# Performance work log

Measured on AMD Instinct MI355X. Metric: run time of the kernel, lower is better.

## Reference

```python
import jax, jax.numpy as jnp
import numpy as np

VOCAB = 30522
PAD_ID = 1  # original skips token id 1


def masked_mean(emb, mask):
    # emb: [..., L, D], mask: [..., L] -> [..., D]
    m = mask.astype(emb.dtype)[..., None]
    s = jnp.sum(emb * m, axis=-2)
    c = jnp.clip(jnp.sum(m, axis=-2), 1.0)
    return s / c


def arg_embedding(tok_ids, sent_ids, emb):
    # tok_ids: [B,S,A,T] int, sent_ids: [B,S,L] int, emb: [B,S,L,D]
    # For each non-pad token: mean of embeddings at all matching sentence
    # positions (0 if no match); then mean over non-pad tokens (0 if none).
    matches = (tok_ids[..., None] == sent_ids[:, :, None, None, :]).astype(emb.dtype)  # [B,S,A,T,L]
    cnt = jnp.clip(jnp.sum(matches, axis=-1, keepdims=True), 1.0)                      # [B,S,A,T,1]
    valid = (tok_ids != PAD_ID).astype(emb.dtype)[..., None]                           # [B,S,A,T,1]
    W = jnp.sum(matches / cnt * valid, axis=3)                                         # [B,S,A,L]
    n_valid = jnp.clip(jnp.sum(valid, axis=(3, 4)), 1.0)[..., None]                    # [B,S,A,1]
    return jnp.einsum('bsal,bsld->bsad', W, emb) / n_valid                             # [B,S,A,D]


def setup_inputs() -> dict:
    key = jax.random.key(0)
    ks = jax.random.split(key, 6)
    B, S, L, D, A, T = 16, 16, 128, 768, 8, 8
    return {
        'sentence_ids': jax.random.randint(ks[0], (B, S, L), 0, VOCAB, dtype=jnp.int64) if jax.config.jax_enable_x64 else jax.random.randint(ks[0], (B, S, L), 0, VOCAB, dtype=jnp.int32),
        'sentence_attention_masks': jax.random.randint(ks[1], (B, S, L), 0, 2, dtype=jnp.int32),
        'sentence_embeddings': jax.random.normal(ks[2], (B, S, L, D), dtype=jnp.float32),
        'predicate_ids': jax.random.randint(ks[3], (B, S, A, T), 0, VOCAB, dtype=jnp.int32),
        'arg0_ids': jax.random.randint(ks[4], (B, S, A, T), 0, VOCAB, dtype=jnp.int32),
        'arg1_ids': jax.random.randint(ks[5], (B, S, A, T), 0, VOCAB, dtype=jnp.int32),
    }


def reference(sentence_ids, sentence_attention_masks, sentence_embeddings,
              predicate_ids, arg0_ids, arg1_ids):
    # sentence_embeddings stands in for bert_model(input_ids, attention_mask)[0]
    sentence_embeddings_avg = masked_mean(sentence_embeddings, sentence_attention_masks)  # [B,S,D]
    predicate_embeddings = arg_embedding(predicate_ids, sentence_ids, sentence_embeddings)
    arg0_embeddings = arg_embedding(arg0_ids, sentence_ids, sentence_embeddings)
    arg1_embeddings = arg_embedding(arg1_ids, sentence_ids, sentence_embeddings)
    return (sentence_embeddings_avg, predicate_embeddings, arg0_embeddings, arg1_embeddings)
```

## Files before the change

### kernel.cpp

```cpp
#include <hip/hip_runtime.h>

#define BB 16
#define SS 16
#define LL 128
#define DD 768
#define AA 8
#define TT 8
#define PAD_ID 1
#define NARG 24
#define NT 768
#define NQ 96
#define NSEG 8
#define SEGL 16
#define CH 2
#define COLS 384

__global__ __launch_bounds__(NT, 8) void srl_kernel(
    const int* __restrict__ sid_g,
    const int* __restrict__ mask_g,
    const float* __restrict__ emb_g,
    const int* __restrict__ pred_g,
    const int* __restrict__ a0_g,
    const int* __restrict__ a1_g,
    float* __restrict__ out)
{
    __shared__ int    sid[LL];
    __shared__ float  maskf[LL];
    __shared__ float  Wt4[LL][4];
    __shared__ float  coeff[NARG][TT];
    __shared__ float  validf[NARG][TT];
    __shared__ int    toks[NARG][TT];
    __shared__ float  inv_msum;
    __shared__ int    amask_sh;
    __shared__ int    nact_sh;
    __shared__ int    actlist[NARG];
    __shared__ int    slotmap[NARG];
    __shared__ float4 P4[NSEG][NQ][4];
    __shared__ float  Wx[LL];

    const int bs  = blockIdx.x;
    const int cc  = blockIdx.y;
    const int tid = threadIdx.x;
    const int q   = tid % NQ;
    const int seg = tid / NQ;

    float* out0 = out;
    float* outA = out + (size_t)BB * SS * DD;
    const int colbase = cc * COLS + 4 * q;

    const float* ep = emb_g + (size_t)bs * (LL * DD)
                    + (size_t)(seg * SEGL) * DD + colbase;
    float4 cur0 = *reinterpret_cast<const float4*>(&ep[0]);
    float4 cur1 = *reinterpret_cast<const float4*>(&ep[DD]);

    if (tid < LL) {
        sid[tid]   = sid_g[bs * LL + tid];
        maskf[tid] = (float)mask_g[bs * LL + tid];
    }
    if (tid == 0) amask_sh = 0;
    __syncthreads();

    if (tid < NARG * TT) {
        const int j = tid >> 3;
        const int t = tid & 7;
        const int k = j >> 3;
        const int a = j & 7;
        const int* src = (k == 0) ? pred_g : (k == 1) ? a0_g : a1_g;
        const int tok = src[bs * AA * TT + a * TT + t];
        int cnt = 0;
        for (int l = 0; l < LL; ++l) cnt += (sid[l] == tok) ? 1 : 0;
        const float v = (tok != PAD_ID) ? 1.0f : 0.0f;
        toks[j][t]   = tok;
        validf[j][t] = v;
        coeff[j][t]  = v / (float)(cnt > 1 ? cnt : 1);
        if (v != 0.0f && cnt > 0) atomicOr(&amask_sh, 1 << j);
    } else if (tid >= 320 && tid < 384) {
        const int lane = tid - 320;
        float s = maskf[lane] + maskf[lane + 64];
        for (int off = 32; off; off >>= 1) s += __shfl_xor(s, off, 64);
        if (lane == 0) inv_msum = 1.0f / fmaxf(s, 1.0f);
    }
    __syncthreads();

    if (tid < NARG) {
        float nv = 0.0f;
        #pragma unroll
        for (int t = 0; t < TT; ++t) nv += validf[tid][t];
        const float inv = 1.0f / fmaxf(nv, 1.0f);
        #pragma unroll
        for (int t = 0; t < TT; ++t) coeff[tid][t] *= inv;
    } else if (tid == NARG) {
        int n = 0;
        const int m = amask_sh;
        for (int j = 0; j < NARG; ++j) {
            slotmap[j] = -1;
            if ((m >> j) & 1) actlist[n++] = j;
        }
        nact_sh = n;
        for (int s = n; s < NARG; ++s) actlist[s] = -1;
        for (int s = 0; s < n && s < 3; ++s) slotmap[actlist[s]] = s + 1;
    }
    __syncthreads();

    if (tid < LL * 4) {
        const int l = tid >> 2;
        const int s = tid & 3;
        float w = 0.0f;
        if (s == 0) {
            w = maskf[l] * inv_msum;
        } else {
            const int j = actlist[s - 1];
            if (j >= 0) {
                const int sl = sid[l];
                #pragma unroll
                for (int t = 0; t < TT; ++t)
                    w += (sl == toks[j][t]) ? coeff[j][t] : 0.0f;
            }
        }
        Wt4[l][s] = w;
    }
    __syncthreads();

    float4 acc0 = make_float4(0.f, 0.f, 0.f, 0.f);
    float4 acc1 = acc0, acc2 = acc0, acc3 = acc0;
    {
        #pragma unroll
        for (int l0 = 0; l0 < SEGL; l0 += CH) {
            float4 nxt0, nxt1;
            if (l0 + CH < SEGL) {
                nxt0 = *reinterpret_cast<const float4*>(&ep[(size_t)(l0 + CH) * DD]);
                nxt1 = *reinterpret_cast<const float4*>(&ep[(size_t)(l0 + CH + 1) * DD]);
            }
            {
                const float4 w = *reinterpret_cast<const float4*>(&Wt4[seg * SEGL + l0][0]);
                const float4 e = cur0;
                acc0.x += w.x * e.x; acc0.y += w.x * e.y; acc0.z += w.x * e.z; acc0.w += w.x * e.w;
                acc1.x += w.y * e.x; acc1.y += w.y * e.y; acc1.z += w.y * e.z; acc1.w += w.y * e.w;
                acc2.x += w.z * e.x; acc2.y += w.z * e.y; acc2.z += w.z * e.z; acc2.w += w.z * e.w;
                acc3.x += w.w * e.x; acc3.y += w.w * e.y; acc3.z += w.w * e.z; acc3.w += w.w * e.w;
            }
            {
                const float4 w = *reinterpret_cast<const float4*>(&Wt4[seg * SEGL + l0 + 1][0]);
                const float4 e = cur1;
                acc0.x += w.x * e.x; acc0.y += w.x * e.y; acc0.z += w.x * e.z; acc0.w += w.x * e.w;
                acc1.x += w.y * e.x; acc1.y += w.y * e.y; acc1.z += w.y * e.z; acc1.w += w.y * e.w;
                acc2.x += w.z * e.x; acc2.y += w.z * e.y; acc2.z += w.z * e.z; acc2.w += w.z * e.w;
                acc3.x += w.w * e.x; acc3.y += w.w * e.y; acc3.z += w.w * e.z; acc3.w += w.w * e.w;
            }
            cur0 = nxt0;
            cur1 = nxt1;
        }
    }
    P4[seg][q][0] = acc0;
    P4[seg][q][1] = acc1;
    P4[seg][q][2] = acc2;
    P4[seg][q][3] = acc3;
    __syncthreads();

    {
        const int g = seg;
        #pragma unroll
        for (int i = 0; i < 4; ++i) {
            const int r = g + 8 * i;
            if (r >= 25) break;
            float4 val = make_float4(0.f, 0.f, 0.f, 0.f);
            int s = -1;
            if (r == 0) s = 0;
            else if (slotmap[r - 1] >= 0) s = slotmap[r - 1];
            if (s >= 0) {
                #pragma unroll
                for (int g2 = 0; g2 < NSEG; ++g2) {
                    const float4 p = P4[g2][q][s];
                    val.x += p.x; val.y += p.y; val.z += p.z; val.w += p.w;
                }
            }
            if (r == 0) {
                *reinterpret_cast<float4*>(&out0[(size_t)bs * DD + colbase]) = val;
            } else {
                const int j = r - 1;
                *reinterpret_cast<float4*>(
                    &outA[(size_t)(j >> 3) * (BB * SS * AA * DD) +
                          ((size_t)bs * AA + (j & 7)) * DD + colbase]) = val;
            }
        }
    }

    for (int e = 3; e < nact_sh; ++e) {
        const int je = actlist[e];
        __syncthreads();
        if (tid < LL) {
            const int sl = sid[tid];
            float w = 0.0f;
            #pragma unroll
            for (int t = 0; t < TT; ++t)
                w += (sl == toks[je][t]) ? coeff[je][t] : 0.0f;
            Wx[tid] = w;
        }
        __syncthreads();
        float4 acc = make_float4(0.f, 0.f, 0.f, 0.f);
        for (int l = 0; l < SEGL; ++l) {
            const float w = Wx[seg * SEGL + l];
            const float4 ev = *reinterpret_cast<const float4*>(&ep[(size_t)l * DD]);
            acc.x += w * ev.x; acc.y += w * ev.y; acc.z += w * ev.z; acc.w += w * ev.w;
        }
        P4[seg][q][0] = acc;
        __syncthreads();
        if (seg == 0) {
            float4 s = make_float4(0.f, 0.f, 0.f, 0.f);
            #pragma unroll
            for (int g2 = 0; g2 < NSEG; ++g2) {
                const float4 p = P4[g2][q][0];
                s.x += p.x; s.y += p.y; s.z += p.z; s.w += p.w;
            }
            *reinterpret_cast<float4*>(
                &outA[(size_t)(je >> 3) * (BB * SS * AA * DD) +
                      ((size_t)bs * AA + (je & 7)) * DD + colbase]) = s;
        }
    }
}

extern "C" void kernel_launch(void* const* d_in, const int* in_sizes, int n_in,
                              void* d_out, int out_size, void* d_ws, size_t ws_size,
                              hipStream_t stream) {
    const int*   sid  = (const int*)d_in[0];
    const int*   mask = (const int*)d_in[1];
    const float* emb  = (const float*)d_in[2];
    const int*   pred = (const int*)d_in[3];
    const int*   a0   = (const int*)d_in[4];
    const int*   a1   = (const int*)d_in[5];
    float* outp = (float*)d_out;

    srl_kernel<<<dim3(BB * SS, DD / COLS), dim3(NT), 0, stream>>>(
        sid, mask, emb, pred, a0, a1, outp);
}
```

Baseline: 29.20 us.

## Split into prep kernel computing weight rows and streaming weighted-sum kernel

Moves token matching, count and coefficient computation and the full weight matrix into a separate prep kernel that writes weights and an active-argument header to workspace. The streaming kernel then only reads precomputed weights and does the embedding accumulation. This removes the duplicated prep work that each column block did before, and it drops the serial prep phase from the bandwidth-bound kernel. The cost is a second launch plus a global round trip for the weights and header. The first kernel's embedding prefetch can no longer overlap the prep work.

After: 32.76 us. +12.2%, slower.

```diff
diff --git a/kernel.cpp b/kernel.cpp
--- a/kernel.cpp
+++ b/kernel.cpp
@@ -8,50 +8,35 @@
 #define TT 8
 #define PAD_ID 1
 #define NARG 24
-#define NT 768
+#define NROW 25
+#define NT1 384
+#define NT2 768
 #define NQ 96
 #define NSEG 8
 #define SEGL 16
-#define CH 2
 #define COLS 384
 
-__global__ __launch_bounds__(NT, 8) void srl_kernel(
+__global__ __launch_bounds__(NT1) void srl_prep(
     const int* __restrict__ sid_g,
     const int* __restrict__ mask_g,
-    const float* __restrict__ emb_g,
     const int* __restrict__ pred_g,
     const int* __restrict__ a0_g,
     const int* __restrict__ a1_g,
-    float* __restrict__ out)
+    float* __restrict__ Wfull,
+    int* __restrict__ hdr)
 {
-    __shared__ int    sid[LL];
-    __shared__ float  maskf[LL];
-    __shared__ float  Wt4[LL][4];
-    __shared__ float  coeff[NARG][TT];
-    __shared__ float  validf[NARG][TT];
-    __shared__ int    toks[NARG][TT];
-    __shared__ float  inv_msum;
-    __shared__ int    amask_sh;
-    __shared__ int    nact_sh;
-    __shared__ int    actlist[NARG];
-    __shared__ int    slotmap[NARG];
-    __shared__ float4 P4[NSEG][NQ][4];
-    __shared__ float  Wx[LL];
+    __shared__ int   sid[LL];
+    __shared__ float maskf[LL];
+    __shared__ float coeff[NARG][TT];
+    __shared__ float validf[NARG][TT];
+    __shared__ int   toks[NARG][TT];
+    __shared__ float inv_msum;
+    __shared__ int   amask_sh;
+    __shared__ int   nact_sh;
+    __shared__ int   actlist[NARG];
 
     const int bs  = blockIdx.x;
-    const int cc  = blockIdx.y;
     const int tid = threadIdx.x;
-    const int q   = tid % NQ;
-    const int seg = tid / NQ;
-
-    float* out0 = out;
-    float* outA = out + (size_t)BB * SS * DD;
-    const int colbase = cc * COLS + 4 * q;
-
-    const float* ep = emb_g + (size_t)bs * (LL * DD)
-                    + (size_t)(seg * SEGL) * DD + colbase;
-    float4 cur0 = *reinterpret_cast<const float4*>(&ep[0]);
-    float4 cur1 = *reinterpret_cast<const float4*>(&ep[DD]);
 
     if (tid < LL) {
         sid[tid]   = sid_g[bs * LL + tid];
@@ -92,64 +77,110 @@
     } else if (tid == NARG) {
         int n = 0;
         const int m = amask_sh;
-        for (int j = 0; j < NARG; ++j) {
-            slotmap[j] = -1;
+        for (int j = 0; j < NARG; ++j)
             if ((m >> j) & 1) actlist[n++] = j;
-        }
         nact_sh = n;
         for (int s = n; s < NARG; ++s) actlist[s] = -1;
-        for (int s = 0; s < n && s < 3; ++s) slotmap[actlist[s]] = s + 1;
-    }
-    __syncthreads();
+    }
+    __syncthreads();
+
+    for (int idx = tid; idx < NROW * LL; idx += NT1) {
+        const int r = idx >> 7;
+        const int l = idx & (LL - 1);
+        float w;
+        if (r == 0) {
+            w = maskf[l] * inv_msum;
+        } else {
+            const int j  = r - 1;
+            const int sl = sid[l];
+            w = 0.0f;
+            #pragma unroll
+            for (int t = 0; t < TT; ++t)
+                w += (sl == toks[j][t]) ? coeff[j][t] : 0.0f;
+        }
+        Wfull[((size_t)bs * NROW + r) * LL + l] = w;
+    }
+    if (tid == NT1 - 1) {
+        hdr[bs * 32] = nact_sh;
+        for (int s = 0; s < NARG; ++s) hdr[bs * 32 + 1 + s] = actlist[s];
+    }
+}
+
+__global__ __launch_bounds__(NT2, 8) void srl_stream(
+    const float* __restrict__ emb_g,
+    const float* __restrict__ Wfull,
+    const int* __restrict__ hdr,
+    float* __restrict__ out)
+{
+    __shared__ float  Wt4[LL][4];
+    __shared__ int    slotmap[NARG];
+    __shared__ int    actlist_sh[NARG];
+    __shared__ int    nact_sh;
+    __shared__ float4 P4[NSEG][NQ][4];
+    __shared__ float  Wx[LL];
+
+    const int bs  = blockIdx.x;
+    const int cc  = blockIdx.y;
+    const int tid = threadIdx.x;
+    const int q   = tid % NQ;
+    const int seg = tid / NQ;
+
+    float* out0 = out;
+    float* outA = out + (size_t)BB * SS * DD;
+    const int colbase = cc * COLS + 4 * q;
+
+    const float* ep = emb_g + (size_t)bs * (LL * DD)
+                    + (size_t)(seg * SEGL) * DD + colbase;
+    float4 cur0 = *reinterpret_cast<const float4*>(&ep[0]);
+    float4 cur1 = *reinterpret_cast<const float4*>(&ep[DD]);
 
     if (tid < LL * 4) {
         const int l = tid >> 2;
         const int s = tid & 3;
-        float w = 0.0f;
+        float w;
         if (s == 0) {
-            w = maskf[l] * inv_msum;
+            w = Wfull[((size_t)bs * NROW) * LL + l];
         } else {
-            const int j = actlist[s - 1];
-            if (j >= 0) {
-                const int sl = sid[l];
-                #pragma unroll
-                for (int t = 0; t < TT; ++t)
-                    w += (sl == toks[j][t]) ? coeff[j][t] : 0.0f;
-            }
+            const int j = hdr[bs * 32 + s];
+            w = (j >= 0) ? Wfull[((size_t)bs * NROW + j + 1) * LL + l] : 0.0f;
         }
         Wt4[l][s] = w;
+    } else if (tid == LL * 4) {
+        const int n = hdr[bs * 32];
+        nact_sh = n;
+        for (int j = 0; j < NARG; ++j) slotmap[j] = -1;
+        for (int s = 0; s < NARG; ++s) actlist_sh[s] = hdr[bs * 32 + 1 + s];
+        for (int s = 0; s < 3 && s < n; ++s) slotmap[actlist_sh[s]] = s + 1;
     }
     __syncthreads();
 
     float4 acc0 = make_float4(0.f, 0.f, 0.f, 0.f);
     float4 acc1 = acc0, acc2 = acc0, acc3 = acc0;
-    {
-        #pragma unroll
-        for (int l0 = 0; l0 < SEGL; l0 += CH) {
-            float4 nxt0, nxt1;
-            if (l0 + CH < SEGL) {
-                nxt0 = *reinterpret_cast<const float4*>(&ep[(size_t)(l0 + CH) * DD]);
-                nxt1 = *reinterpret_cast<const float4*>(&ep[(size_t)(l0 + CH + 1) * DD]);
-            }
-            {
-                const float4 w = *reinterpret_cast<const float4*>(&Wt4[seg * SEGL + l0][0]);
-                const float4 e = cur0;
-                acc0.x += w.x * e.x; acc0.y += w.x * e.y; acc0.z += w.x * e.z; acc0.w += w.x * e.w;
-                acc1.x += w.y * e.x; acc1.y += w.y * e.y; acc1.z += w.y * e.z; acc1.w += w.y * e.w;
-                acc2.x += w.z * e.x; acc2.y += w.z * e.y; acc2.z += w.z * e.z; acc2.w += w.z * e.w;
-                acc3.x += w.w * e.x; acc3.y += w.w * e.y; acc3.z += w.w * e.z; acc3.w += w.w * e.w;
-            }
-            {
-                const float4 w = *reinterpret_cast<const float4*>(&Wt4[seg * SEGL + l0 + 1][0]);
-                const float4 e = cur1;
-                acc0.x += w.x * e.x; acc0.y += w.x * e.y; acc0.z += w.x * e.z; acc0.w += w.x * e.w;
-                acc1.x += w.y * e.x; acc1.y += w.y * e.y; acc1.z += w.y * e.z; acc1.w += w.y * e.w;
-                acc2.x += w.z * e.x; acc2.y += w.z * e.y; acc2.z += w.z * e.z; acc2.w += w.z * e.w;
-                acc3.x += w.w * e.x; acc3.y += w.w * e.y; acc3.z += w.w * e.z; acc3.w += w.w * e.w;
-            }
-            cur0 = nxt0;
-            cur1 = nxt1;
-        }
+    #pragma unroll
+    for (int l0 = 0; l0 < SEGL; l0 += 2) {
+        float4 nxt0, nxt1;
+        if (l0 + 2 < SEGL) {
+            nxt0 = *reinterpret_cast<const float4*>(&ep[(size_t)(l0 + 2) * DD]);
+            nxt1 = *reinterpret_cast<const float4*>(&ep[(size_t)(l0 + 3) * DD]);
+        }
+        {
+            const float4 w = *reinterpret_cast<const float4*>(&Wt4[seg * SEGL + l0][0]);
+            const float4 e = cur0;
+            acc0.x += w.x * e.x; acc0.y += w.x * e.y; acc0.z += w.x * e.z; acc0.w += w.x * e.w;
+            acc1.x += w.y * e.x; acc1.y += w.y * e.y; acc1.z += w.y * e.z; acc1.w += w.y * e.w;
+            acc2.x += w.z * e.x; acc2.y += w.z * e.y; acc2.z += w.z * e.z; acc2.w += w.z * e.w;
+            acc3.x += w.w * e.x; acc3.y += w.w * e.y; acc3.z += w.w * e.z; acc3.w += w.w * e.w;
+        }
+        {
+            const float4 w = *reinterpret_cast<const float4*>(&Wt4[seg * SEGL + l0 + 1][0]);
+            const float4 e = cur1;
+            acc0.x += w.x * e.x; acc0.y += w.x * e.y; acc0.z += w.x * e.z; acc0.w += w.x * e.w;
+            acc1.x += w.y * e.x; acc1.y += w.y * e.y; acc1.z += w.y * e.z; acc1.w += w.y * e.w;
+            acc2.x += w.z * e.x; acc2.y += w.z * e.y; acc2.z += w.z * e.z; acc2.w += w.z * e.w;
+            acc3.x += w.w * e.x; acc3.y += w.w * e.y; acc3.z += w.w * e.z; acc3.w += w.w * e.w;
+        }
+        cur0 = nxt0;
+        cur1 = nxt1;
     }
     P4[seg][q][0] = acc0;
     P4[seg][q][1] = acc1;
@@ -162,7 +193,7 @@
         #pragma unroll
         for (int i = 0; i < 4; ++i) {
             const int r = g + 8 * i;
-            if (r >= 25) break;
+            if (r >= NROW) break;
             float4 val = make_float4(0.f, 0.f, 0.f, 0.f);
             int s = -1;
             if (r == 0) s = 0;
@@ -186,16 +217,10 @@
     }
 
     for (int e = 3; e < nact_sh; ++e) {
-        const int je = actlist[e];
+        const int je = actlist_sh[e];
         __syncthreads();
-        if (tid < LL) {
-            const int sl = sid[tid];
-            float w = 0.0f;
-            #pragma unroll
-            for (int t = 0; t < TT; ++t)
-                w += (sl == toks[je][t]) ? coeff[je][t] : 0.0f;
-            Wx[tid] = w;
-        }
+        if (tid < LL)
+            Wx[tid] = Wfull[((size_t)bs * NROW + je + 1) * LL + tid];
         __syncthreads();
         float4 acc = make_float4(0.f, 0.f, 0.f, 0.f);
         for (int l = 0; l < SEGL; ++l) {
@@ -230,6 +255,11 @@
     const int*   a1   = (const int*)d_in[5];
     float* outp = (float*)d_out;
 
-    srl_kernel<<<dim3(BB * SS, DD / COLS), dim3(NT), 0, stream>>>(
-        sid, mask, emb, pred, a0, a1, outp);
+    float* Wfull = (float*)d_ws;
+    int*   hdr   = (int*)((char*)d_ws + (size_t)BB * SS * NROW * LL * sizeof(float));
+
+    srl_prep<<<dim3(BB * SS), dim3(NT1), 0, stream>>>(
+        sid, mask, pred, a0, a1, Wfull, hdr);
+    srl_stream<<<dim3(BB * SS, DD / COLS), dim3(NT2), 0, stream>>>(
+        emb, Wfull, hdr, outp);
 }
```
